# Optimization experiments

Measured on AMD Instinct MI355X. Metric: run time of the kernel, lower is better.

## Reference

```python
import jax, jax.numpy as jnp
import numpy as np


def _mine_domain(emb, labels):
    """emb: [B, F] float, labels: [B] int.
    Returns hardest-positive / hardest-negative sims and embeddings."""
    B = emb.shape[0]
    sim = emb @ emb.T                                  # [B, B]
    eq = labels[:, None] == labels[None, :]            # same-label mask
    same = eq & ~jnp.eye(B, dtype=bool)                # positives (exclude self)
    diff = ~eq                                         # negatives
    pos_sim = jnp.where(same, sim, jnp.inf)            # mask non-positives
    neg_sim = jnp.where(diff, sim, -jnp.inf)           # mask non-negatives
    min_sim = jnp.min(pos_sim, axis=1)                 # smallest pos similarity
    min_idx = jnp.argmin(pos_sim, axis=1)
    max_sim = jnp.max(neg_sim, axis=1)                 # largest neg similarity
    max_idx = jnp.argmax(neg_sim, axis=1)
    has_pos = jnp.any(same, axis=1)                    # rows with >=1 positive
    zero = jnp.zeros((), dtype=emb.dtype)
    pdist = jnp.where(has_pos, min_sim, zero)
    ndist = jnp.where(has_pos, max_sim, zero)
    pembed = jnp.where(has_pos[:, None], emb[min_idx], zero)  # [B, F]
    nembed = jnp.where(has_pos[:, None], emb[max_idx], zero)  # [B, F]
    return pdist, ndist, pembed, nembed


def setup_inputs() -> dict:
    key = jax.random.key(0)
    k1, k2 = jax.random.split(key)
    D, B, F = 4, 8192, 128
    semb = jax.random.normal(k1, (D, B, F), dtype=jnp.float32)
    slabels = jax.random.randint(k2, (D, B), 0, 64, dtype=jnp.int64)
    return {"semb": semb, "slabels": slabels}


def reference(semb, slabels):
    # vmap over the independent domains
    pos_dist, neg_dist, pos_embed, neg_embed = jax.vmap(_mine_domain)(semb, slabels)
    return pos_dist, neg_dist, pos_embed, neg_embed
```

## Files before the change

### kernel.cpp

```cpp
#include <hip/hip_runtime.h>
#include <limits.h>
#include <math.h>
#include <stdint.h>

constexpr int D_ = 4;
constexpr int B_ = 8192;
constexpr int F_ = 128;
constexpr int BM = 64;
constexpr int BN = 64;
constexpr int NCT = B_ / BN;
constexpr float LO_SCALE = 4096.f;
constexpr float LO_INV = 1.f / 4096.f;

typedef _Float16 f16x8 __attribute__((ext_vector_type(8)));
typedef float f32x16 __attribute__((ext_vector_type(16)));

__device__ __host__ constexpr int ROFS(int reg) { return (reg & 3) + 8 * (reg >> 2); }

__global__ __launch_bounds__(256)
void convert_f16(const float* __restrict__ src,
                 _Float16* __restrict__ hi, _Float16* __restrict__ lo) {
    const size_t i0 = ((size_t)blockIdx.x * 256 + threadIdx.x) * 8;
    const float4 a = *(const float4*)(src + i0);
    const float4 b = *(const float4*)(src + i0 + 4);
    const float xs[8] = {a.x, a.y, a.z, a.w, b.x, b.y, b.z, b.w};
    f16x8 h, l;
    #pragma unroll
    for (int k = 0; k < 8; ++k) {
        const _Float16 hh = (_Float16)xs[k];
        h[k] = hh;
        l[k] = (_Float16)((xs[k] - (float)hh) * LO_SCALE);
    }
    *(f16x8*)(hi + i0) = h;
    *(f16x8*)(lo + i0) = l;
}

template <bool PRE>
__global__ __launch_bounds__(256, 2)
void mine_mfma(const float* __restrict__ emb,
               const _Float16* __restrict__ Ehi,
               const _Float16* __restrict__ Elo,
               const int* __restrict__ labels,
               float* __restrict__ out) {
    __shared__ f16x8 BhiS[1024];
    __shared__ f16x8 BloS[1024];
    __shared__ float mrgF[2][2][16][4];
    __shared__ int   rowinfo[64][2];

    const int tid = threadIdx.x;
    const int lane = tid & 63;
    const int wid = tid >> 6;
    const int wr = wid >> 1, wc = wid & 1;
    const int l31 = lane & 31, h = lane >> 5;

    const int bid = blockIdx.x;
    const int d = bid >> 7;
    const int rt = bid & 127;
    const int row0 = rt * BM;

    const float* __restrict__ embD = emb + (size_t)d * B_ * F_;
    const _Float16* __restrict__ EhiD = Ehi + (size_t)d * B_ * F_;
    const _Float16* __restrict__ EloD = Elo + (size_t)d * B_ * F_;
    const int* __restrict__ labD = labels + d * B_;

    const int arow = row0 + wr * 32 + l31;
    f16x8 Ah[8], Al[8];
    #pragma unroll
    for (int ks = 0; ks < 8; ++ks) {
        if constexpr (PRE) {
            Ah[ks] = *(const f16x8*)(EhiD + (size_t)arow * F_ + ks * 16 + h * 8);
            Al[ks] = *(const f16x8*)(EloD + (size_t)arow * F_ + ks * 16 + h * 8);
        } else {
            const float* p = embD + (size_t)arow * F_ + ks * 16 + h * 8;
            const float4 x = *(const float4*)p;
            const float4 y = *(const float4*)(p + 4);
            const float xs[8] = {x.x, x.y, x.z, x.w, y.x, y.y, y.z, y.w};
            #pragma unroll
            for (int k = 0; k < 8; ++k) {
                const _Float16 hh = (_Float16)xs[k];
                Ah[ks][k] = hh;
                Al[ks][k] = (_Float16)((xs[k] - (float)hh) * LO_SCALE);
            }
        }
    }

    const int rbase = row0 + wr * 32 + 4 * h;
    int rlab[16];
    #pragma unroll
    for (int reg = 0; reg < 16; ++reg) rlab[reg] = labD[rbase + ROFS(reg)];

    float pmin[16], nmax[16];
    int pidx[16], nidx[16];
    #pragma unroll
    for (int reg = 0; reg < 16; ++reg) {
        pmin[reg] = INFINITY;  pidx[reg] = INT_MAX;
        nmax[reg] = -INFINITY; nidx[reg] = INT_MAX;
    }

    int sr[4], sg[4], sslot[4];
    #pragma unroll
    for (int i = 0; i < 4; ++i) {
        const int flat = i * 256 + tid;
        sr[i] = flat >> 4;
        sg[i] = flat & 15;
        sslot[i] = sr[i] * 16 + (sg[i] ^ (sr[i] & 15));
    }

    f16x8 sh[4], sl[4];
    auto loadStage = [&](int ct) {
        #pragma unroll
        for (int i = 0; i < 4; ++i) {
            if constexpr (PRE) {
                sh[i] = *(const f16x8*)(EhiD + (size_t)(ct * 64 + sr[i]) * F_ + sg[i] * 8);
                sl[i] = *(const f16x8*)(EloD + (size_t)(ct * 64 + sr[i]) * F_ + sg[i] * 8);
            } else {
                const float* p = embD + (size_t)(ct * 64 + sr[i]) * F_ + sg[i] * 8;
                const float4 x = *(const float4*)p;
                const float4 y = *(const float4*)(p + 4);
                const float xs[8] = {x.x, x.y, x.z, x.w, y.x, y.y, y.z, y.w};
                #pragma unroll
                for (int k = 0; k < 8; ++k) {
                    const _Float16 hh = (_Float16)xs[k];
                    sh[i][k] = hh;
                    sl[i][k] = (_Float16)((xs[k] - (float)hh) * LO_SCALE);
                }
            }
        }
    };
    auto writeStage = [&]() {
        #pragma unroll
        for (int i = 0; i < 4; ++i) {
            BhiS[sslot[i]] = sh[i];
            BloS[sslot[i]] = sl[i];
        }
    };

    const int brow = wc * 32 + l31;
    const int bswz = brow & 15;

    loadStage(0);
    for (int ct = 0; ct < NCT; ++ct) {
        __syncthreads();
        writeStage();
        __syncthreads();
        if (ct + 1 < NCT) loadStage(ct + 1);

        f32x16 a1, a2;
        #pragma unroll
        for (int r = 0; r < 16; ++r) { a1[r] = 0.f; a2[r] = 0.f; }

        #pragma unroll
        for (int ks = 0; ks < 8; ++ks) {
            const int g = 2 * ks + h;
            const f16x8 bh = BhiS[brow * 16 + (g ^ bswz)];
            const f16x8 bl = BloS[brow * 16 + (g ^ bswz)];
            a1 = __builtin_amdgcn_mfma_f32_32x32x16_f16(Ah[ks], bh, a1, 0, 0, 0);
            a2 = __builtin_amdgcn_mfma_f32_32x32x16_f16(Ah[ks], bl, a2, 0, 0, 0);
            a2 = __builtin_amdgcn_mfma_f32_32x32x16_f16(Al[ks], bh, a2, 0, 0, 0);
        }

        const int jl = ct * 64 + brow;
        const int cl = labD[jl];

        if (ct == rt) {
            #pragma unroll
            for (int reg = 0; reg < 16; ++reg) {
                const float s = fmaf(a2[reg], LO_INV, a1[reg]);
                const bool same = (cl == rlab[reg]);
                const bool self = (jl == rbase + ROFS(reg));
                const float ps = (same && !self) ? s : INFINITY;
                if (ps < pmin[reg]) { pmin[reg] = ps; pidx[reg] = jl; }
                const float ns = same ? -INFINITY : s;
                if (ns > nmax[reg]) { nmax[reg] = ns; nidx[reg] = jl; }
            }
        } else {
            #pragma unroll
            for (int reg = 0; reg < 16; ++reg) {
                const float s = fmaf(a2[reg], LO_INV, a1[reg]);
                const bool same = (cl == rlab[reg]);
                const float ps = same ? INFINITY : s;
                const float ns = same ? -INFINITY : s;
                const float pp = same ? s : INFINITY;
                if (pp < pmin[reg]) { pmin[reg] = pp; pidx[reg] = jl; }
                if (ns > nmax[reg]) { nmax[reg] = ns; nidx[reg] = jl; }
                (void)ps;
            }
        }
    }

    #pragma unroll
    for (int off = 1; off < 32; off <<= 1)
        #pragma unroll
        for (int reg = 0; reg < 16; ++reg) {
            float ov = __shfl_xor(pmin[reg], off);
            int oi = __shfl_xor(pidx[reg], off);
            if (ov < pmin[reg]) { pmin[reg] = ov; pidx[reg] = oi; }
            ov = __shfl_xor(nmax[reg], off);
            oi = __shfl_xor(nidx[reg], off);
            if (ov > nmax[reg]) { nmax[reg] = ov; nidx[reg] = oi; }
        }

    __syncthreads();
    if (wc == 1) {
        #pragma unroll
        for (int reg = 0; reg < 16; ++reg)
            if (l31 == reg) {
                mrgF[wr][h][reg][0] = pmin[reg];
                mrgF[wr][h][reg][1] = __int_as_float(pidx[reg]);
                mrgF[wr][h][reg][2] = nmax[reg];
                mrgF[wr][h][reg][3] = __int_as_float(nidx[reg]);
            }
    }
    __syncthreads();

    float* __restrict__ pd = out;
    float* __restrict__ nd = out + (size_t)D_ * B_;
    float* __restrict__ pe = out + (size_t)2 * D_ * B_;
    float* __restrict__ ne = pe + (size_t)D_ * B_ * F_;

    if (wc == 0) {
        #pragma unroll
        for (int reg = 0; reg < 16; ++reg) {
            const float ov = mrgF[wr][h][reg][0];
            const int oi = __float_as_int(mrgF[wr][h][reg][1]);
            if (ov < pmin[reg]) { pmin[reg] = ov; pidx[reg] = oi; }
            const float on = mrgF[wr][h][reg][2];
            const int oni = __float_as_int(mrgF[wr][h][reg][3]);
            if (on > nmax[reg]) { nmax[reg] = on; nidx[reg] = oni; }
        }
        #pragma unroll
        for (int reg = 0; reg < 16; ++reg)
            if (l31 == reg) {
                const int rib = wr * 32 + 4 * h + ROFS(reg);
                const bool has = (pidx[reg] != INT_MAX);
                const size_t grow = (size_t)d * B_ + row0 + rib;
                pd[grow] = has ? pmin[reg] : 0.f;
                nd[grow] = has ? nmax[reg] : 0.f;
                rowinfo[rib][0] = has ? pidx[reg] : -1;
                rowinfo[rib][1] = (nidx[reg] == INT_MAX) ? 0 : nidx[reg];
            }
    }
    __syncthreads();

    {
        const int r = tid >> 2;
        const int part = tid & 3;
        const int pi = rowinfo[r][0];
        const int ni = rowinfo[r][1];
        const size_t ob = ((size_t)d * B_ + row0 + r) * F_ + part * 32;
        const float4 zv = make_float4(0.f, 0.f, 0.f, 0.f);
        const float4* sp = (const float4*)(embD + (size_t)(pi < 0 ? 0 : pi) * F_ + part * 32);
        const float4* sn = (const float4*)(embD + (size_t)ni * F_ + part * 32);
        #pragma unroll
        for (int q = 0; q < 8; ++q) {
            *(float4*)(&pe[ob + q * 4]) = (pi >= 0) ? sp[q] : zv;
            *(float4*)(&ne[ob + q * 4]) = (pi >= 0) ? sn[q] : zv;
        }
    }
}

extern "C" void kernel_launch(void* const* d_in, const int* in_sizes, int n_in,
                              void* d_out, int out_size, void* d_ws, size_t ws_size,
                              hipStream_t stream) {
    const float* emb = (const float*)d_in[0];
    const int* labels = (const int*)d_in[1];
    float* out = (float*)d_out;

    const size_t NE = (size_t)D_ * B_ * F_;
    const bool ws_ok = ws_size >= NE * 2 * sizeof(_Float16);

    if (ws_ok) {
        _Float16* Ehi = (_Float16*)d_ws;
        _Float16* Elo = Ehi + NE;
        convert_f16<<<dim3((unsigned)(NE / 2048)), 256, 0, stream>>>(emb, Ehi, Elo);
        mine_mfma<true><<<dim3(D_ * (B_ / BM)), 256, 0, stream>>>(emb, Ehi, Elo, labels, out);
    } else {
        mine_mfma<false><<<dim3(D_ * (B_ / BM)), 256, 0, stream>>>(emb, nullptr, nullptr, labels, out);
    }
}
```

Before: 614.7 us.

## Split column tiles across three blocks and merge partial argmin/argmax in separate kernel

Each row tile now processes only a third of the column tiles, tripling the grid so more CUs stay busy. Per-part hardest positive/negative values and indices are written as packed tuples to workspace, and a new merge_gather kernel reduces them and gathers the selected embeddings. Row labels are packed into bytes and the diagonal special case is folded into one loop. This adds an extra launch and workspace traffic, and relies on labels fitting in 8 bits and indices in 16 bits.

```diff
diff --git a/kernel.cpp b/kernel.cpp
--- a/kernel.cpp
+++ b/kernel.cpp
@@ -9,6 +9,8 @@
 constexpr int BM = 64;
 constexpr int BN = 64;
 constexpr int NCT = B_ / BN;
+constexpr int NPARTS = 3;
+constexpr int TPP = 43;
 constexpr float LO_SCALE = 4096.f;
 constexpr float LO_INV = 1.f / 4096.f;
 
@@ -36,16 +38,14 @@
 }
 
 template <bool PRE>
-__global__ __launch_bounds__(256, 2)
+__global__ __launch_bounds__(256, 3)
 void mine_mfma(const float* __restrict__ emb,
                const _Float16* __restrict__ Ehi,
                const _Float16* __restrict__ Elo,
                const int* __restrict__ labels,
-               float* __restrict__ out) {
+               uint4* __restrict__ tuples) {
     __shared__ f16x8 BhiS[1024];
     __shared__ f16x8 BloS[1024];
-    __shared__ float mrgF[2][2][16][4];
-    __shared__ int   rowinfo[64][2];
 
     const int tid = threadIdx.x;
     const int lane = tid & 63;
@@ -54,9 +54,14 @@
     const int l31 = lane & 31, h = lane >> 5;
 
     const int bid = blockIdx.x;
-    const int d = bid >> 7;
-    const int rt = bid & 127;
+    const int p = bid >> 9;
+    const int r9 = bid & 511;
+    const int d = r9 >> 7;
+    const int rt = r9 & 127;
     const int row0 = rt * BM;
+
+    const int ct0 = p * TPP;
+    const int ct1 = (ct0 + TPP < NCT) ? ct0 + TPP : NCT;
 
     const float* __restrict__ embD = emb + (size_t)d * B_ * F_;
     const _Float16* __restrict__ EhiD = Ehi + (size_t)d * B_ * F_;
@@ -71,9 +76,9 @@
             Ah[ks] = *(const f16x8*)(EhiD + (size_t)arow * F_ + ks * 16 + h * 8);
             Al[ks] = *(const f16x8*)(EloD + (size_t)arow * F_ + ks * 16 + h * 8);
         } else {
-            const float* p = embD + (size_t)arow * F_ + ks * 16 + h * 8;
-            const float4 x = *(const float4*)p;
-            const float4 y = *(const float4*)(p + 4);
+            const float* pp = embD + (size_t)arow * F_ + ks * 16 + h * 8;
+            const float4 x = *(const float4*)pp;
+            const float4 y = *(const float4*)(pp + 4);
             const float xs[8] = {x.x, x.y, x.z, x.w, y.x, y.y, y.z, y.w};
             #pragma unroll
             for (int k = 0; k < 8; ++k) {
@@ -85,9 +90,15 @@
     }
 
     const int rbase = row0 + wr * 32 + 4 * h;
-    int rlab[16];
-    #pragma unroll
-    for (int reg = 0; reg < 16; ++reg) rlab[reg] = labD[rbase + ROFS(reg)];
+    uint32_t rlab4[4];
+    #pragma unroll
+    for (int q = 0; q < 4; ++q) {
+        uint32_t v = 0;
+        #pragma unroll
+        for (int j = 0; j < 4; ++j)
+            v |= ((uint32_t)labD[rbase + 8 * q + j] & 0xFFu) << (8 * j);
+        rlab4[q] = v;
+    }
 
     float pmin[16], nmax[16];
     int pidx[16], nidx[16];
@@ -114,9 +125,9 @@
                 sh[i] = *(const f16x8*)(EhiD + (size_t)(ct * 64 + sr[i]) * F_ + sg[i] * 8);
                 sl[i] = *(const f16x8*)(EloD + (size_t)(ct * 64 + sr[i]) * F_ + sg[i] * 8);
             } else {
-                const float* p = embD + (size_t)(ct * 64 + sr[i]) * F_ + sg[i] * 8;
-                const float4 x = *(const float4*)p;
-                const float4 y = *(const float4*)(p + 4);
+                const float* pp = embD + (size_t)(ct * 64 + sr[i]) * F_ + sg[i] * 8;
+                const float4 x = *(const float4*)pp;
+                const float4 y = *(const float4*)(pp + 4);
                 const float xs[8] = {x.x, x.y, x.z, x.w, y.x, y.y, y.z, y.w};
                 #pragma unroll
                 for (int k = 0; k < 8; ++k) {
@@ -138,16 +149,16 @@
     const int brow = wc * 32 + l31;
     const int bswz = brow & 15;
 
-    loadStage(0);
-    for (int ct = 0; ct < NCT; ++ct) {
+    loadStage(ct0);
+    for (int ct = ct0; ct < ct1; ++ct) {
         __syncthreads();
         writeStage();
         __syncthreads();
-        if (ct + 1 < NCT) loadStage(ct + 1);
+        if (ct + 1 < ct1) loadStage(ct + 1);
 
         f32x16 a1, a2;
         #pragma unroll
-        for (int r = 0; r < 16; ++r) { a1[r] = 0.f; a2[r] = 0.f; }
+        for (int q = 0; q < 16; ++q) { a1[q] = 0.f; a2[q] = 0.f; }
 
         #pragma unroll
         for (int ks = 0; ks < 8; ++ks) {
@@ -160,31 +171,17 @@
         }
 
         const int jl = ct * 64 + brow;
-        const int cl = labD[jl];
-
-        if (ct == rt) {
-            #pragma unroll
-            for (int reg = 0; reg < 16; ++reg) {
-                const float s = fmaf(a2[reg], LO_INV, a1[reg]);
-                const bool same = (cl == rlab[reg]);
-                const bool self = (jl == rbase + ROFS(reg));
-                const float ps = (same && !self) ? s : INFINITY;
-                if (ps < pmin[reg]) { pmin[reg] = ps; pidx[reg] = jl; }
-                const float ns = same ? -INFINITY : s;
-                if (ns > nmax[reg]) { nmax[reg] = ns; nidx[reg] = jl; }
-            }
-        } else {
-            #pragma unroll
-            for (int reg = 0; reg < 16; ++reg) {
-                const float s = fmaf(a2[reg], LO_INV, a1[reg]);
-                const bool same = (cl == rlab[reg]);
-                const float ps = same ? INFINITY : s;
-                const float ns = same ? -INFINITY : s;
-                const float pp = same ? s : INFINITY;
-                if (pp < pmin[reg]) { pmin[reg] = pp; pidx[reg] = jl; }
-                if (ns > nmax[reg]) { nmax[reg] = ns; nidx[reg] = jl; }
-                (void)ps;
-            }
+        const uint32_t clb = (uint32_t)labD[jl] & 0xFFu;
+
+        #pragma unroll
+        for (int reg = 0; reg < 16; ++reg) {
+            const float s = fmaf(a2[reg], LO_INV, a1[reg]);
+            const bool same = (((rlab4[reg >> 2] >> ((reg & 3) * 8)) & 0xFFu) == clb);
+            const bool self = (jl == rbase + ROFS(reg));
+            const float ps = (same && !self) ? s : INFINITY;
+            if (ps < pmin[reg]) { pmin[reg] = ps; pidx[reg] = jl; }
+            const float ns = same ? -INFINITY : s;
+            if (ns > nmax[reg]) { nmax[reg] = ns; nidx[reg] = jl; }
         }
     }
 
@@ -200,62 +197,76 @@
             if (ov > nmax[reg]) { nmax[reg] = ov; nidx[reg] = oi; }
         }
 
-    __syncthreads();
-    if (wc == 1) {
-        #pragma unroll
-        for (int reg = 0; reg < 16; ++reg)
-            if (l31 == reg) {
-                mrgF[wr][h][reg][0] = pmin[reg];
-                mrgF[wr][h][reg][1] = __int_as_float(pidx[reg]);
-                mrgF[wr][h][reg][2] = nmax[reg];
-                mrgF[wr][h][reg][3] = __int_as_float(nidx[reg]);
-            }
-    }
-    __syncthreads();
+    #pragma unroll
+    for (int reg = 0; reg < 16; ++reg) {
+        if (l31 == reg) {
+            const int row = rbase + ROFS(reg);
+            const uint32_t pi = (pidx[reg] == INT_MAX) ? 0xFFFFu : (uint32_t)pidx[reg];
+            const uint32_t ni = (nidx[reg] == INT_MAX) ? 0xFFFFu : (uint32_t)nidx[reg];
+            uint4 t;
+            t.x = __float_as_uint(pmin[reg]);
+            t.y = __float_as_uint(nmax[reg]);
+            t.z = pi | (ni << 16);
+            t.w = 0u;
+            tuples[(((size_t)d * B_ + row) * NPARTS + p) * 2 + wc] = t;
+        }
+    }
+}
+
+__global__ __launch_bounds__(256)
+void merge_gather(const float* __restrict__ emb,
+                  const uint4* __restrict__ tuples,
+                  float* __restrict__ out) {
+    const int tid = threadIdx.x;
+    const int g = tid & 15;
+    const int grp = tid >> 4;
+    const int rowg = blockIdx.x * 16 + grp;
+    const int d = rowg >> 13;
+
+    float pmin = INFINITY, nmax = -INFINITY;
+    int pidx = -1, nidx = -1;
+    #pragma unroll
+    for (int t = 0; t < NPARTS * 2; ++t) {
+        const uint4 tp = tuples[(size_t)rowg * (NPARTS * 2) + t];
+        const float pv = __uint_as_float(tp.x);
+        const float nv = __uint_as_float(tp.y);
+        const int pi = (int)(tp.z & 0xFFFFu);
+        const int ni = (int)(tp.z >> 16);
+        if (pi != 0xFFFF && (pidx < 0 || pv < pmin || (pv == pmin && pi < pidx))) {
+            pmin = pv; pidx = pi;
+        }
+        if (ni != 0xFFFF && (nidx < 0 || nv > nmax || (nv == nmax && ni < nidx))) {
+            nmax = nv; nidx = ni;
+        }
+    }
 
     float* __restrict__ pd = out;
     float* __restrict__ nd = out + (size_t)D_ * B_;
     float* __restrict__ pe = out + (size_t)2 * D_ * B_;
     float* __restrict__ ne = pe + (size_t)D_ * B_ * F_;
 
-    if (wc == 0) {
-        #pragma unroll
-        for (int reg = 0; reg < 16; ++reg) {
-            const float ov = mrgF[wr][h][reg][0];
-            const int oi = __float_as_int(mrgF[wr][h][reg][1]);
-            if (ov < pmin[reg]) { pmin[reg] = ov; pidx[reg] = oi; }
-            const float on = mrgF[wr][h][reg][2];
-            const int oni = __float_as_int(mrgF[wr][h][reg][3]);
-            if (on > nmax[reg]) { nmax[reg] = on; nidx[reg] = oni; }
-        }
-        #pragma unroll
-        for (int reg = 0; reg < 16; ++reg)
-            if (l31 == reg) {
-                const int rib = wr * 32 + 4 * h + ROFS(reg);
-                const bool has = (pidx[reg] != INT_MAX);
-                const size_t grow = (size_t)d * B_ + row0 + rib;
-                pd[grow] = has ? pmin[reg] : 0.f;
-                nd[grow] = has ? nmax[reg] : 0.f;
-                rowinfo[rib][0] = has ? pidx[reg] : -1;
-                rowinfo[rib][1] = (nidx[reg] == INT_MAX) ? 0 : nidx[reg];
-            }
-    }
-    __syncthreads();
-
-    {
-        const int r = tid >> 2;
-        const int part = tid & 3;
-        const int pi = rowinfo[r][0];
-        const int ni = rowinfo[r][1];
-        const size_t ob = ((size_t)d * B_ + row0 + r) * F_ + part * 32;
+    const bool has = (pidx >= 0);
+    if (g == 0) {
+        pd[rowg] = has ? pmin : 0.f;
+        nd[rowg] = has ? nmax : 0.f;
+    }
+
+    const float* __restrict__ embD = emb + (size_t)d * B_ * F_;
+    const size_t ob = (size_t)rowg * F_;
+    if (has) {
+        const int ni2 = (nidx < 0) ? 0 : nidx;
+        const float4* sp = (const float4*)(embD + (size_t)pidx * F_);
+        const float4* sn = (const float4*)(embD + (size_t)ni2 * F_);
+        *(float4*)(&pe[ob + g * 4]) = sp[g];
+        *(float4*)(&pe[ob + 64 + g * 4]) = sp[16 + g];
+        *(float4*)(&ne[ob + g * 4]) = sn[g];
+        *(float4*)(&ne[ob + 64 + g * 4]) = sn[16 + g];
+    } else {
         const float4 zv = make_float4(0.f, 0.f, 0.f, 0.f);
-        const float4* sp = (const float4*)(embD + (size_t)(pi < 0 ? 0 : pi) * F_ + part * 32);
-        const float4* sn = (const float4*)(embD + (size_t)ni * F_ + part * 32);
-        #pragma unroll
-        for (int q = 0; q < 8; ++q) {
-            *(float4*)(&pe[ob + q * 4]) = (pi >= 0) ? sp[q] : zv;
-            *(float4*)(&ne[ob + q * 4]) = (pi >= 0) ? sn[q] : zv;
-        }
+        *(float4*)(&pe[ob + g * 4]) = zv;
+        *(float4*)(&pe[ob + 64 + g * 4]) = zv;
+        *(float4*)(&ne[ob + g * 4]) = zv;
+        *(float4*)(&ne[ob + 64 + g * 4]) = zv;
     }
 }
 
@@ -267,14 +278,20 @@
     float* out = (float*)d_out;
 
     const size_t NE = (size_t)D_ * B_ * F_;
-    const bool ws_ok = ws_size >= NE * 2 * sizeof(_Float16);
-
-    if (ws_ok) {
-        _Float16* Ehi = (_Float16*)d_ws;
+    const size_t TUP_BYTES = (size_t)D_ * B_ * NPARTS * 2 * 16;
+    uint4* tuples = (uint4*)d_ws;
+
+    const bool pre_ok = ws_size >= TUP_BYTES + NE * 2 * sizeof(_Float16);
+
+    if (pre_ok) {
+        _Float16* Ehi = (_Float16*)((char*)d_ws + TUP_BYTES);
         _Float16* Elo = Ehi + NE;
         convert_f16<<<dim3((unsigned)(NE / 2048)), 256, 0, stream>>>(emb, Ehi, Elo);
-        mine_mfma<true><<<dim3(D_ * (B_ / BM)), 256, 0, stream>>>(emb, Ehi, Elo, labels, out);
+        mine_mfma<true><<<dim3(NPARTS * D_ * (B_ / BM)), 256, 0, stream>>>(
+            emb, Ehi, Elo, labels, tuples);
     } else {
-        mine_mfma<false><<<dim3(D_ * (B_ / BM)), 256, 0, stream>>>(emb, nullptr, nullptr, labels, out);
-    }
-}
+        mine_mfma<false><<<dim3(NPARTS * D_ * (B_ / BM)), 256, 0, stream>>>(
+            emb, nullptr, nullptr, labels, tuples);
+    }
+    merge_gather<<<dim3(D_ * B_ / 16), 256, 0, stream>>>(emb, tuples, out);
+}
```

Result: slower. 1.228 ms (+99.7%).
